# Kernel optimization log

Measured on AMD Instinct MI355X. Metric: run time of the kernel, lower is better.

## Reference

```python
import jax, jax.numpy as jnp
import numpy as np

B, T, D, H, K, ED = 4, 1024, 512, 8, 30, 128
HD = D // H
SCALE = HD ** -0.5


def _ln(x, g, b, eps=1e-5):
    m = jnp.mean(x, axis=-1, keepdims=True)
    v = jnp.var(x, axis=-1, keepdims=True)
    return (x - m) / jnp.sqrt(v + eps) * g + b


def setup_inputs() -> dict:
    key = jax.random.key(0)
    ks = jax.random.split(key, 16)
    s = 0.02
    return {
        "h_V": jax.random.normal(ks[0], (B, T, D), jnp.float32),
        "k": jax.random.normal(ks[1], (B, T, D), jnp.float32),
        "v": jax.random.normal(ks[2], (B, T, D), jnp.float32),
        "E": jax.random.normal(ks[3], (B, T, K, ED), jnp.float32),
        "bias": jax.random.normal(ks[4], (B, T, T), jnp.float32),
        "Wq": jax.random.normal(ks[5], (D, D), jnp.float32) * s,
        "bq": jnp.zeros((D,), jnp.float32),
        "Wk": jax.random.normal(ks[6], (D, D), jnp.float32) * s,
        "bk": jnp.zeros((D,), jnp.float32),
        "Wv": jax.random.normal(ks[7], (D, D), jnp.float32) * s,
        "bv": jnp.zeros((D,), jnp.float32),
        "Wo": jax.random.normal(ks[8], (D, D + ED), jnp.float32) * s,
        "bo": jnp.zeros((D,), jnp.float32),
        "t": jax.random.normal(ks[9], (1,), jnp.float32),
        "gn": jnp.ones((D,), jnp.float32),
        "bn": jnp.zeros((D,), jnp.float32),
        "w1": jax.random.normal(ks[10], (4 * D, D), jnp.float32) * s,
        "bw1": jnp.zeros((4 * D,), jnp.float32),
        "w2": jax.random.normal(ks[11], (D, 4 * D), jnp.float32) * s,
        "bw2": jnp.zeros((D,), jnp.float32),
        "gf": jnp.ones((D,), jnp.float32),
        "bf": jnp.zeros((D,), jnp.float32),
        "g2": jnp.ones((D,), jnp.float32),
        "b2": jnp.zeros((D,), jnp.float32),
        "E_idx": jax.random.randint(ks[12], (B, T, K), 0, T),
        "mask": jax.random.randint(ks[13], (B, T), 0, 2).astype(jnp.int32),
    }


def reference(h_V, k, v, E, bias, Wq, bq, Wk, bk, Wv, bv, Wo, bo, t, gn, bn, w1, bw1, w2, bw2, gf, bf, g2, b2, E_idx, mask):
    # q/k/v projections; q scaled by head_dim**-0.5 (as in torch: q *= scaling)
    q = (h_V @ Wq.T + bq) * SCALE
    kk = k @ Wk.T + bk
    vv = v @ Wv.T + bv
    qh = q.reshape(B, T, H, HD)
    kh = kk.reshape(B, T, H, HD)
    vh = vv.reshape(B, T, H, HD)
    # attention logits with additive pairwise bias, broadcast over heads
    aw = jnp.einsum('bthd,bshd->bhts', qh, kh) + bias[:, None, :, :]
    aw = jnp.where(mask[:, None, None, :] == 0, -1e9, aw)
    # h_attend temperature scaling
    aw = aw / (4.0 ** jnp.tanh(t[0]))
    p = jax.nn.softmax(aw, axis=-1)  # [B,H,T,S]
    attn = jnp.einsum('bhts,bshd->bthd', p, vh).reshape(B, T, D)
    # edge path: head-mean attention, gather neighbor weights, weighted edge sum
    ma = jnp.mean(p, axis=1)                       # [B,T,S]
    g = jnp.take_along_axis(ma, E_idx, axis=-1)    # [B,T,K]
    edge = (g[..., None] * E).sum(axis=2) / (g.sum(axis=-1, keepdims=True) + 1e-6)  # [B,T,ED]
    out = jnp.concatenate([attn, edge], axis=-1) @ Wo.T + bo
    h = _ln(h_V + out, gn, bn, eps=1e-5)
    # PositionwiseFeedForward: residual + LN(eps=1e-6)
    ff = jax.nn.gelu(h @ w1.T + bw1, approximate=False) @ w2.T + bw2
    dh = _ln(h + ff, gf, bf, eps=1e-6)
    return _ln(h + dh, g2, b2, eps=1e-5)
```

## Files before the change

### kernel.cpp

```cpp
#include <hip/hip_runtime.h>
#include <hip/hip_fp16.h>
#include <math.h>

#define B_ 4
#define T_ 1024
#define D_ 512
#define H_ 8
#define HD_ 64
#define KN 30
#define ED_ 128
#define DFF_ 2048
#define M_ 4096
#define BH_ 32

typedef _Float16 f16;
typedef __attribute__((ext_vector_type(8))) _Float16 f16x8;
typedef __attribute__((ext_vector_type(4))) _Float16 f16x4;
typedef __attribute__((ext_vector_type(4))) float f32x4;

#define MFMA16 __builtin_amdgcn_mfma_f32_16x16x32_f16
#define LOG2E 1.44269504088896f

__device__ __forceinline__ f16x8 ld8(const f16* p){ return *reinterpret_cast<const f16x8*>(p); }

__device__ __forceinline__ void gld16(const void* g, void* l){
  __builtin_amdgcn_global_load_lds((const __attribute__((address_space(1))) void*)g,
                                   (__attribute__((address_space(3))) void*)l, 16, 0, 0);
}

struct CvtJobs {
  const float* s[9];
  f16* d[9];
  int start[10];
};

__global__ __launch_bounds__(256) void cvt9_kernel(CvtJobs J){
  const int blk = blockIdx.x;
  int j = 0;
  while (j < 8 && blk >= J.start[j+1]) ++j;
  const int i = (blk - J.start[j])*256 + threadIdx.x;
  float4 v = reinterpret_cast<const float4*>(J.s[j])[i];
  union { f16 h[4]; ushort4 u; } o;
  o.h[0]=(f16)v.x; o.h[1]=(f16)v.y; o.h[2]=(f16)v.z; o.h[3]=(f16)v.w;
  reinterpret_cast<ushort4*>(J.d[j])[i] = o.u;
}

__global__ __launch_bounds__(256) void biasprep_kernel(
    const float* __restrict__ bias, const int* __restrict__ mask,
    const float* __restrict__ tsc, f16* __restrict__ biasT)
{
  const int TT = blockIdx.x*256 + threadIdx.x;
  const int G = TT >> 4, l16 = TT & 15;
  const int qg = G & 1, step = (G >> 1) & 1, ws = (G >> 2) & 3;
  const int c = (G >> 4) & 7, tb = (G >> 7) & 31, bi = G >> 12;
  const float s = exp2f(-2.0f*tanhf(tsc[0]))*LOG2E;
  const int t  = tb*32 + qg*16 + l16;
  const int s0 = c*128 + ws*32 + step*16;
  const float* bp = bias + ((size_t)bi*T_ + t)*T_ + s0;
  const int*   mp = mask + bi*T_ + s0;
  union { f16 h[16]; f16x8 v8[2]; } o;
#pragma unroll
  for (int i = 0; i < 16; i += 4){
    float4 v = *reinterpret_cast<const float4*>(bp + i);
    int4  mm = *reinterpret_cast<const int4*>(mp + i);
    float x[4] = {v.x,v.y,v.z,v.w};
    int  m4[4] = {mm.x,mm.y,mm.z,mm.w};
#pragma unroll
    for (int j = 0; j < 4; ++j){
      float tv = (x[j] + (m4[j] ? 0.f : -60000.f))*s;
      o.h[i+j] = (f16)fmaxf(tv, -60000.f);
    }
  }
  f16* op = biasT + (size_t)G*256 + l16*16;
  reinterpret_cast<f16x8*>(op)[0] = o.v8[0];
  reinterpret_cast<f16x8*>(op)[1] = o.v8[1];
}

template<int EPI>
__global__ __launch_bounds__(256,2) void gemm_tile(
    const f16* __restrict__ X, const f16* __restrict__ W,
    const float* __restrict__ bias, void* __restrict__ outp,
    int Kd, int ldo, int nbN)
{
  __shared__ f16 As[128*64];
  __shared__ f16 Bs[128*64];
  const int nwg = gridDim.x;
  const int bid = blockIdx.x;
  const int swz = (bid & 7)*(nwg >> 3) + (bid >> 3);
  const int mb = swz / nbN, nb = swz - mb*nbN;
  const int rb = mb*128, cb = nb*128;
  const int tid = threadIdx.x;
  const int w = tid >> 6, lane = tid & 63;
  const int l16 = lane & 15, l4 = lane >> 4;
  const int wr = w >> 1, wc = w & 1;
  const int key = l16 & 7;

  f32x4 acc[4][4];
#pragma unroll
  for (int m = 0; m < 4; ++m)
#pragma unroll
    for (int n = 0; n < 4; ++n) acc[m][n] = (f32x4){0.f,0.f,0.f,0.f};

  for (int k0 = 0; k0 < Kd; k0 += 64){
#pragma unroll
    for (int i = 0; i < 4; ++i){
      const int cidx = i*256 + w*64 + lane;
      const int r = cidx >> 3, p = cidx & 7;
      gld16(X + (size_t)(rb + r)*Kd + k0 + ((p ^ (r & 7)) << 3),
            &As[(i*256 + w*64)*8]);
      gld16(W + (size_t)(cb + r)*Kd + k0 + ((p ^ (r & 7)) << 3),
            &Bs[(i*256 + w*64)*8]);
    }
    __syncthreads();
#pragma unroll
    for (int kk = 0; kk < 2; ++kk){
      f16x8 a[4], b[4];
#pragma unroll
      for (int m = 0; m < 4; ++m)
        a[m] = ld8(&As[(wr*64 + m*16 + l16)*64 + (((kk*4 + l4) ^ key) << 3)]);
#pragma unroll
      for (int n = 0; n < 4; ++n)
        b[n] = ld8(&Bs[(wc*64 + n*16 + l16)*64 + (((kk*4 + l4) ^ key) << 3)]);
#pragma unroll
      for (int m = 0; m < 4; ++m)
#pragma unroll
        for (int n = 0; n < 4; ++n)
          acc[m][n] = MFMA16(a[m], b[n], acc[m][n], 0,0,0);
    }
    __syncthreads();
  }

#pragma unroll
  for (int n = 0; n < 4; ++n){
    const int col = cb + wc*64 + n*16 + l16;
    const float bv = bias[col];
#pragma unroll
    for (int m = 0; m < 4; ++m){
#pragma unroll
      for (int j = 0; j < 4; ++j){
        const int row = rb + wr*64 + m*16 + l4*4 + j;
        float v = acc[m][n][j] + bv;
        if (EPI == 1){
          v = 0.5f*v*(1.0f + erff(v*0.70710678118654752f));
          ((f16*)outp)[(size_t)row*ldo + col] = (f16)v;
        } else {
          ((float*)outp)[(size_t)row*ldo + col] = v;
        }
      }
    }
  }
}

template<int EPI>
__global__ __launch_bounds__(256,2) void gemm_n64(
    const f16* __restrict__ X, const f16* __restrict__ W,
    const float* __restrict__ bias, void* __restrict__ outp,
    int Kd, int ldo, int nbN)
{
  __shared__ f16 As[128*64];
  __shared__ f16 Bs[64*64];
  const int nwg = gridDim.x;
  const int bid = blockIdx.x;
  const int swz = (bid & 7)*(nwg >> 3) + (bid >> 3);
  const int mb = swz / nbN, nb = swz - mb*nbN;
  const int rb = mb*128, cb = nb*64;
  const int tid = threadIdx.x;
  const int w = tid >> 6, lane = tid & 63;
  const int l16 = lane & 15, l4 = lane >> 4;
  const int wr = w >> 1, wc = w & 1;
  const int key = l16 & 7;

  f32x4 acc[4][2];
#pragma unroll
  for (int m = 0; m < 4; ++m)
#pragma unroll
    for (int n = 0; n < 2; ++n) acc[m][n] = (f32x4){0.f,0.f,0.f,0.f};

  for (int k0 = 0; k0 < Kd; k0 += 64){
#pragma unroll
    for (int i = 0; i < 4; ++i){
      const int cidx = i*256 + w*64 + lane;
      const int r = cidx >> 3, p = cidx & 7;
      gld16(X + (size_t)(rb + r)*Kd + k0 + ((p ^ (r & 7)) << 3),
            &As[(i*256 + w*64)*8]);
    }
#pragma unroll
    for (int i = 0; i < 2; ++i){
      const int cidx = i*256 + w*64 + lane;
      const int r = cidx >> 3, p = cidx & 7;
      gld16(W + (size_t)(cb + r)*Kd + k0 + ((p ^ (r & 7)) << 3),
            &Bs[(i*256 + w*64)*8]);
    }
    __syncthreads();
#pragma unroll
    for (int kk = 0; kk < 2; ++kk){
      f16x8 a[4], b[2];
#pragma unroll
      for (int m = 0; m < 4; ++m)
        a[m] = ld8(&As[(wr*64 + m*16 + l16)*64 + (((kk*4 + l4) ^ key) << 3)]);
#pragma unroll
      for (int n = 0; n < 2; ++n)
        b[n] = ld8(&Bs[(wc*32 + n*16 + l16)*64 + (((kk*4 + l4) ^ key) << 3)]);
#pragma unroll
      for (int m = 0; m < 4; ++m)
#pragma unroll
        for (int n = 0; n < 2; ++n)
          acc[m][n] = MFMA16(a[m], b[n], acc[m][n], 0,0,0);
    }
    __syncthreads();
  }

#pragma unroll
  for (int n = 0; n < 2; ++n){
    const int col = cb + wc*32 + n*16 + l16;
    const float bv = bias[col];
#pragma unroll
    for (int m = 0; m < 4; ++m){
#pragma unroll
      for (int j = 0; j < 4; ++j){
        const int row = rb + wr*64 + m*16 + l4*4 + j;
        float v = acc[m][n][j] + bv;
        if (EPI == 1){
          v = 0.5f*v*(1.0f + erff(v*0.70710678118654752f));
          ((f16*)outp)[(size_t)row*ldo + col] = (f16)v;
        } else {
          ((float*)outp)[(size_t)row*ldo + col] = v;
        }
      }
    }
  }
}

__global__ __launch_bounds__(256,2) void qkv_tile(
    const f16* __restrict__ hV, const f16* __restrict__ kI, const f16* __restrict__ vI,
    const f16* __restrict__ Wq, const f16* __restrict__ Wk, const f16* __restrict__ Wv,
    const float* __restrict__ bq, const float* __restrict__ bk, const float* __restrict__ bv,
    const float* __restrict__ tsc,
    f16* __restrict__ qo, f16* __restrict__ ko, f16* __restrict__ vT)
{
  __shared__ f16 As[128*32];
  __shared__ f16 Bs[128*32];
  const int bid = blockIdx.x;
  const int swz = (bid & 7)*48 + (bid >> 3);
  const int g = swz >> 7;
  const int r = swz & 127;
  const int mb = r >> 2, nb = r & 3;
  const f16* X  = (g == 0) ? hV : ((g == 1) ? kI : vI);
  const f16* W  = (g == 0) ? Wq : ((g == 1) ? Wk : Wv);
  const float* bias = (g == 0) ? bq : ((g == 1) ? bk : bv);
  const int rb = mb*128, cb = nb*128;
  const int tid = threadIdx.x;
  const int w = tid >> 6, lane = tid & 63;
  const int l16 = lane & 15, l4 = lane >> 4;
  const int wr = w >> 1, wc = w & 1;
  const int sr = lane >> 2, sc = (lane & 3)*8;
  const f16* Ax0 = X + (size_t)(rb + w*16 + sr)*D_ + sc;
  const f16* Ax1 = X + (size_t)(rb + 64 + w*16 + sr)*D_ + sc;
  const f16* Bx0 = W + (size_t)(cb + w*16 + sr)*D_ + sc;
  const f16* Bx1 = W + (size_t)(cb + 64 + w*16 + sr)*D_ + sc;
  f16* Ad0 = &As[(w*16)*32];
  f16* Ad1 = &As[(64 + w*16)*32];
  f16* Bd0 = &Bs[(w*16)*32];
  f16* Bd1 = &Bs[(64 + w*16)*32];

  f32x4 acc[4][4];
#pragma unroll
  for (int m = 0; m < 4; ++m)
#pragma unroll
    for (int n = 0; n < 4; ++n) acc[m][n] = (f32x4){0.f,0.f,0.f,0.f};

  for (int k0 = 0; k0 < D_; k0 += 32){
    gld16(Ax0 + k0, Ad0);
    gld16(Ax1 + k0, Ad1);
    gld16(Bx0 + k0, Bd0);
    gld16(Bx1 + k0, Bd1);
    __syncthreads();
    f16x8 a[4], b[4];
#pragma unroll
    for (int m = 0; m < 4; ++m) a[m] = ld8(&As[(wr*64 + m*16 + l16)*32 + l4*8]);
#pragma unroll
    for (int n = 0; n < 4; ++n) b[n] = ld8(&Bs[(wc*64 + n*16 + l16)*32 + l4*8]);
#pragma unroll
    for (int m = 0; m < 4; ++m)
#pragma unroll
      for (int n = 0; n < 4; ++n)
        acc[m][n] = MFMA16(a[m], b[n], acc[m][n], 0,0,0);
    __syncthreads();
  }

  const float qs = exp2f(-2.0f*tanhf(tsc[0]))*LOG2E*0.125f;
  const float scale = (g == 0) ? qs : 1.0f;
  f16* out = (g == 0) ? qo : ko;
#pragma unroll
  for (int n = 0; n < 4; ++n){
    const int col = cb + wc*64 + n*16 + l16;
    const float bv = bias[col];
#pragma unroll
    for (int m = 0; m < 4; ++m){
#pragma unroll
      for (int j = 0; j < 4; ++j){
        const int row = rb + wr*64 + m*16 + l4*4 + j;
        const float v = (acc[m][n][j] + bv)*scale;
        if (g < 2){
          out[(size_t)row*D_ + col] = (f16)v;
        } else {
          const int b = row >> 10, t = row & (T_-1);
          const int h = col >> 6,  dl = col & (HD_-1);
          vT[(((size_t)b*H_ + h)*HD_ + dl)*T_ + t] = (f16)v;
        }
      }
    }
  }
}

__global__ __launch_bounds__(512,4) void attn_fused(
    const f16* __restrict__ q, const f16* __restrict__ k, const f16* __restrict__ vT,
    const f16* __restrict__ biasT, const int* __restrict__ eidx,
    f16* __restrict__ X2, float* __restrict__ gpart)
{
  __shared__ f16 Sb[16384];
  __shared__ f16 Pc[32*128];
  const int bid = blockIdx.x;
  const int swz = (bid & 7)*128 + (bid >> 3);
  const int bh = swz >> 5, tb = swz & 31;
  const int bi = bh >> 3, h = bh & 7;
  const int t0 = tb*32;
  const int tid = threadIdx.x, w = tid >> 6, lane = tid & 63;
  const int qg = w >> 2, ws = w & 3;
  const int l16 = lane & 15, l4 = lane >> 4;
  const int key = l16 & 7;

  const f16* qp = q + (size_t)(bi*T_ + t0 + qg*16 + l16)*D_ + h*HD_ + l4*8;
  const f16x8 q0 = ld8(qp), q1 = ld8(qp + 32);
  const int tl = tid & 255;
  int ga_r, ga_kk, ga_id, gb_r = 0, gb_kk = 0, gb_id = -1;
  ga_r = tl/KN; ga_kk = tl - ga_r*KN;
  ga_id = eidx[((size_t)(bi*T_ + t0 + qg*16 + ga_r))*KN + ga_kk];
  if (tl + 256 < 16*KN){
    gb_r = (tl+256)/KN; gb_kk = (tl+256) - gb_r*KN;
    gb_id = eidx[((size_t)(bi*T_ + t0 + qg*16 + gb_r))*KN + gb_kk];
  }

  const f16* kg = k + (size_t)(bi*T_)*D_ + h*HD_;
  const f16* vg = vT + (size_t)bh*HD_*T_;
  const f16* bb = biasT + (size_t)(bi*32 + tb)*32768 + ws*1024 + qg*256 + l16*16 + l4*4;

  auto stageK = [&](int c, int slot){
#pragma unroll
    for (int i = 0; i < 2; ++i){
      const int cidx = i*512 + w*64 + lane;
      const int r = cidx >> 3, p = cidx & 7;
      gld16(kg + (size_t)(c*128 + r)*D_ + ((p ^ (r & 7)) << 3),
            &Sb[slot*8192 + (i*512 + w*64)*8]);
    }
  };
  auto stageV = [&](int sc, int slot){
#pragma unroll
    for (int i = 0; i < 2; ++i){
      const int cidx = i*512 + w*64 + lane;
      const int r = cidx >> 4, p = cidx & 15;
      gld16(vg + (size_t)r*T_ + sc*128 + ((p ^ (r & 7)) << 3),
            &Sb[slot*8192 + (i*512 + w*64)*8]);
    }
  };

  f32x4 acc[16];
  stageK(0, 0);
#pragma unroll
  for (int c = 0; c < 8; ++c){
    if (c < 7) stageK(c+1, (c+1)&1);
    if (c < 7) asm volatile("s_waitcnt vmcnt(2)" ::: "memory");
    else       asm volatile("s_waitcnt vmcnt(0)" ::: "memory");
    __builtin_amdgcn_sched_barrier(0);
    __builtin_amdgcn_s_barrier();
    __builtin_amdgcn_sched_barrier(0);
    const int base = (c&1)*8192;
#pragma unroll
    for (int step = 0; step < 2; ++step){
      const int rr = ws*32 + step*16 + l16;
      f32x4 a = {0.f,0.f,0.f,0.f};
      a = MFMA16(ld8(&Sb[base + rr*64 + ((l4 ^ key) << 3)]),       q0, a, 0,0,0);
      a = MFMA16(ld8(&Sb[base + rr*64 + (((4 + l4) ^ key) << 3)]), q1, a, 0,0,0);
      const f16x4 bf = *reinterpret_cast<const f16x4*>(bb + c*4096 + step*512);
#pragma unroll
      for (int j = 0; j < 4; ++j) a[j] += (float)bf[j];
      acc[c*2 + step] = a;
    }
    __builtin_amdgcn_s_barrier();
  }

  float* redf = (float*)Sb;
  float m = -3.4e38f;
#pragma unroll
  for (int c = 0; c < 16; ++c)
#pragma unroll
    for (int j = 0; j < 4; ++j) m = fmaxf(m, acc[c][j]);
  m = fmaxf(m, __shfl_xor(m, 16));
  m = fmaxf(m, __shfl_xor(m, 32));
  if (lane < 16) redf[(qg*4 + ws)*16 + lane] = m;
  __syncthreads();
  m = fmaxf(fmaxf(redf[(qg*4+0)*16 + l16], redf[(qg*4+1)*16 + l16]),
            fmaxf(redf[(qg*4+2)*16 + l16], redf[(qg*4+3)*16 + l16]));
  float l = 0.f;
#pragma unroll
  for (int c = 0; c < 16; ++c)
#pragma unroll
    for (int j = 0; j < 4; ++j){
      const float e = exp2f(acc[c][j] - m);
      l += e;
      acc[c][j] = e;
    }
  l += __shfl_xor(l, 16);
  l += __shfl_xor(l, 32);
  if (lane < 16) redf[128 + (qg*4 + ws)*16 + lane] = l;
  __syncthreads();
  const float lrq = redf[128 + (qg*4+0)*16 + l16] + redf[128 + (qg*4+1)*16 + l16]
                  + redf[128 + (qg*4+2)*16 + l16] + redf[128 + (qg*4+3)*16 + l16];
  __syncthreads();
  const float lr_a = __shfl(lrq, ga_r);
  const float lr_b = __shfl(lrq, gb_r);

  f32x4 oo0 = {0.f,0.f,0.f,0.f}, oo1 = oo0, oo2 = oo0, oo3 = oo0;
  stageV(0, 0);
#pragma unroll
  for (int sc = 0; sc < 8; ++sc){
#pragma unroll
    for (int step = 0; step < 2; ++step){
      const int slb = ws*32 + step*16 + l4*4;
      f16x4 pp;
#pragma unroll
      for (int j = 0; j < 4; ++j) pp[j] = (f16)acc[sc*2 + step][j];
      *reinterpret_cast<f16x4*>(
          &Pc[(qg*16 + l16)*128 + (((slb >> 3) ^ key) << 3) + (slb & 7)]) = pp;
    }
    if (sc < 7) stageV(sc+1, (sc+1)&1);
    if (sc < 7) asm volatile("s_waitcnt vmcnt(2) lgkmcnt(0)" ::: "memory");
    else        asm volatile("s_waitcnt vmcnt(0) lgkmcnt(0)" ::: "memory");
    __builtin_amdgcn_sched_barrier(0);
    __builtin_amdgcn_s_barrier();
    __builtin_amdgcn_sched_barrier(0);
    const int base = (sc&1)*8192;
    const int vrow = (ws*16 + l16)*128;
#pragma unroll
    for (int grp = 0; grp < 4; ++grp){
      const int ch = (grp*4 + l4) ^ key;
      const f16x8 pa = ld8(&Pc[(qg*16 + l16)*128 + (ch << 3)]);
      const f16x8 vb = ld8(&Sb[base + vrow + (ch << 3)]);
      if (grp == 0)      oo0 = MFMA16(pa, vb, oo0, 0,0,0);
      else if (grp == 1) oo1 = MFMA16(pa, vb, oo1, 0,0,0);
      else if (grp == 2) oo2 = MFMA16(pa, vb, oo2, 0,0,0);
      else               oo3 = MFMA16(pa, vb, oo3, 0,0,0);
    }
    if ((ga_id >> 7) == sc){
      const int r = qg*16 + ga_r;
      const int sl = ga_id & 127;
      const float pv = (float)Pc[r*128 + ((((sl >> 3) ^ (r & 7)) << 3) | (sl & 7))];
      gpart[((size_t)bh*T_ + t0 + r)*KN + ga_kk] = pv/lr_a*0.125f;
    }
    if (gb_id >= 0 && (gb_id >> 7) == sc){
      const int r = qg*16 + gb_r;
      const int sl = gb_id & 127;
      const float pv = (float)Pc[r*128 + ((((sl >> 3) ^ (r & 7)) << 3) | (sl & 7))];
      gpart[((size_t)bh*T_ + t0 + r)*KN + gb_kk] = pv/lr_b*0.125f;
    }
    __builtin_amdgcn_s_barrier();
  }
  const f32x4 o = (oo0 + oo1) + (oo2 + oo3);

#pragma unroll
  for (int j = 0; j < 4; ++j){
    const float lr = __shfl(lrq, l4*4 + j);
    const int t = t0 + qg*16 + l4*4 + j;
    X2[((size_t)(bi*T_ + t))*640 + h*HD_ + ws*16 + l16] = (f16)(o[j]/lr);
  }
}

__global__ __launch_bounds__(128) void edge_kernel(
    const float* __restrict__ gpart, const float* __restrict__ E, f16* __restrict__ X2)
{
  __shared__ float gl[KN];
  __shared__ float ginv;
  const int bt = blockIdx.x;
  const int bi = bt >> 10, tt = bt & 1023;
  const int t = threadIdx.x;
  if (t < KN){
    float s = 0.f;
#pragma unroll
    for (int hh = 0; hh < H_; ++hh)
      s += gpart[((size_t)(bi*H_ + hh)*T_ + tt)*KN + t];
    gl[t] = s;
  }
  __syncthreads();
  if (t == 0){
    float s = 0.f;
#pragma unroll
    for (int i = 0; i < KN; ++i) s += gl[i];
    ginv = 1.0f/(s + 1e-6f);
  }
  __syncthreads();
  float acc = 0.f;
  const float* Ep = E + (size_t)bt*KN*ED_ + t;
#pragma unroll 5
  for (int kk = 0; kk < KN; ++kk) acc += gl[kk]*Ep[(size_t)kk*ED_];
  X2[(size_t)bt*640 + 512 + t] = (f16)(acc*ginv);
}

__device__ __forceinline__ float block_sum(float v, float* sbuf){
  for (int o = 32; o; o >>= 1) v += __shfl_down(v, o);
  __syncthreads();
  if ((threadIdx.x & 63) == 0) sbuf[threadIdx.x >> 6] = v;
  __syncthreads();
  return sbuf[0]+sbuf[1]+sbuf[2]+sbuf[3];
}

__global__ __launch_bounds__(256) void ln1_kernel(
    const float* __restrict__ hV, const float* __restrict__ hraw,
    const float* __restrict__ gn, const float* __restrict__ bn,
    float* __restrict__ hf, f16* __restrict__ hh)
{
  __shared__ float sbuf[4];
  const int r = blockIdx.x, t = threadIdx.x;
  const size_t base = (size_t)r*D_;
  float x0 = hV[base+t]     + hraw[base+t];
  float x1 = hV[base+t+256] + hraw[base+t+256];
  float s = block_sum(x0+x1, sbuf);
  const float mean = s*(1.f/512.f);
  float d0 = x0-mean, d1 = x1-mean;
  float vs = block_sum(d0*d0+d1*d1, sbuf);
  const float rstd = rsqrtf(vs*(1.f/512.f) + 1e-5f);
  float y0 = d0*rstd*gn[t]     + bn[t];
  float y1 = d1*rstd*gn[t+256] + bn[t+256];
  hf[base+t]     = y0;  hh[base+t]     = (f16)y0;
  hf[base+t+256] = y1;  hh[base+t+256] = (f16)y1;
}

__global__ __launch_bounds__(256) void final_kernel(
    const float* __restrict__ hf, const float* __restrict__ ffr,
    const float* __restrict__ gf, const float* __restrict__ bfv,
    const float* __restrict__ g2, const float* __restrict__ b2,
    float* __restrict__ out)
{
  __shared__ float sbuf[4];
  const int r = blockIdx.x, t = threadIdx.x;
  const size_t base = (size_t)r*D_;
  const float h0 = hf[base+t], h1 = hf[base+t+256];
  float x0 = h0 + ffr[base+t], x1 = h1 + ffr[base+t+256];
  float s = block_sum(x0+x1, sbuf);
  float mean = s*(1.f/512.f);
  float d0 = x0-mean, d1 = x1-mean;
  float vs = block_sum(d0*d0+d1*d1, sbuf);
  float rstd = rsqrtf(vs*(1.f/512.f) + 1e-6f);
  const float dh0 = d0*rstd*gf[t]     + bfv[t];
  const float dh1 = d1*rstd*gf[t+256] + bfv[t+256];
  const float y0 = h0 + dh0, y1 = h1 + dh1;
  s = block_sum(y0+y1, sbuf);
  mean = s*(1.f/512.f);
  d0 = y0-mean; d1 = y1-mean;
  vs = block_sum(d0*d0+d1*d1, sbuf);
  rstd = rsqrtf(vs*(1.f/512.f) + 1e-5f);
  out[base+t]     = d0*rstd*g2[t]     + b2[t];
  out[base+t+256] = d1*rstd*g2[t+256] + b2[t+256];
}

extern "C" void kernel_launch(void* const* d_in, const int* in_sizes, int n_in,
                              void* d_out, int out_size, void* d_ws, size_t ws_size,
                              hipStream_t stream)
{
  (void)in_sizes; (void)n_in; (void)out_size;
  const float* h_V  = (const float*)d_in[0];
  const float* kin  = (const float*)d_in[1];
  const float* vin  = (const float*)d_in[2];
  const float* E    = (const float*)d_in[3];
  const float* bias = (const float*)d_in[4];
  const float* Wq   = (const float*)d_in[5];
  const float* bq   = (const float*)d_in[6];
  const float* Wk   = (const float*)d_in[7];
  const float* bk   = (const float*)d_in[8];
  const float* Wv   = (const float*)d_in[9];
  const float* bv   = (const float*)d_in[10];
  const float* Wo   = (const float*)d_in[11];
  const float* bo   = (const float*)d_in[12];
  const float* tsc  = (const float*)d_in[13];
  const float* gn   = (const float*)d_in[14];
  const float* bn   = (const float*)d_in[15];
  const float* w1   = (const float*)d_in[16];
  const float* bw1  = (const float*)d_in[17];
  const float* w2   = (const float*)d_in[18];
  const float* bw2  = (const float*)d_in[19];
  const float* gf   = (const float*)d_in[20];
  const float* bfv  = (const float*)d_in[21];
  const float* g2   = (const float*)d_in[22];
  const float* b2   = (const float*)d_in[23];
  const int*   Eidx = (const int*)d_in[24];
  const int*   mask = (const int*)d_in[25];
  float* out = (float*)d_out;

  char* wsb = (char*)d_ws;
  size_t off = 0;
  auto alloc = [&](size_t bytes) -> void* {
    void* pp = wsb + off; off += (bytes + 255) & ~(size_t)255; return pp;
  };
  f16* hVb  = (f16*)alloc((size_t)M_*D_*2);
  f16* kbI  = (f16*)alloc((size_t)M_*D_*2);
  f16* vbI  = (f16*)alloc((size_t)M_*D_*2);
  f16* Wqb  = (f16*)alloc((size_t)D_*D_*2);
  f16* Wkb  = (f16*)alloc((size_t)D_*D_*2);
  f16* Wvb  = (f16*)alloc((size_t)D_*D_*2);
  f16* Wob  = (f16*)alloc((size_t)D_*(D_+ED_)*2);
  f16* w1b  = (f16*)alloc((size_t)DFF_*D_*2);
  f16* w2b  = (f16*)alloc((size_t)D_*DFF_*2);
  f16* qb   = (f16*)alloc((size_t)M_*D_*2);
  f16* kb   = (f16*)alloc((size_t)M_*D_*2);
  f16* vT   = (f16*)alloc((size_t)M_*D_*2);
  f16* biasT= (f16*)alloc((size_t)B_*T_*T_*2);
  f16* X2   = (f16*)alloc((size_t)M_*640*2);
  float* gpart = (float*)alloc((size_t)BH_*T_*KN*4);
  float* hraw = (float*)alloc((size_t)M_*D_*4);
  float* hf   = (float*)alloc((size_t)M_*D_*4);
  f16*   hh   = (f16*)alloc((size_t)M_*D_*2);
  f16*   ff1  = (f16*)alloc((size_t)M_*DFF_*2);
  if (ws_size < off) return;
  float* ffraw = hraw;

  {
    CvtJobs J;
    const float* srcs[9] = {h_V, kin, vin, Wq, Wk, Wv, Wo, w1, w2};
    f16* dsts[9] = {hVb, kbI, vbI, Wqb, Wkb, Wvb, Wob, w1b, w2b};
    const int n4s[9] = {M_*D_/4, M_*D_/4, M_*D_/4, D_*D_/4, D_*D_/4, D_*D_/4,
                        D_*(D_+ED_)/4, DFF_*D_/4, D_*DFF_/4};
    int cum = 0;
    for (int i = 0; i < 9; ++i){
      J.s[i] = srcs[i]; J.d[i] = dsts[i]; J.start[i] = cum;
      cum += n4s[i]/256;
    }
    J.start[9] = cum;
    cvt9_kernel<<<cum,256,0,stream>>>(J);
  }
  biasprep_kernel<<<1024,256,0,stream>>>(bias, mask, tsc, biasT);

  qkv_tile<<<384,256,0,stream>>>(hVb, kbI, vbI, Wqb, Wkb, Wvb, bq, bk, bv, tsc, qb, kb, vT);

  attn_fused<<<1024,512,0,stream>>>(qb, kb, vT, biasT, Eidx, X2, gpart);

  edge_kernel<<<M_,128,0,stream>>>(gpart, E, X2);

  gemm_n64<2><<<256,256,0,stream>>>(X2, Wob, bo, hraw, D_+ED_, D_, 8);
  ln1_kernel<<<M_,256,0,stream>>>(h_V, hraw, gn, bn, hf, hh);

  gemm_tile<1><<<512,256,0,stream>>>(hh, w1b, bw1, ff1, D_, DFF_, 16);
  gemm_n64<2><<<256,256,0,stream>>>(ff1, w2b, bw2, ffraw, DFF_, D_, 8);

  final_kernel<<<M_,256,0,stream>>>(hf, ffraw, gf, bfv, g2, b2, out);
}
```

Before: 168.1 us.

## Prefetch bias fragments, defer gpart stores, and store GEMM/LN intermediates in fp16

The bias prep kernel is re-laid-out so each thread writes one 8-wide fp16 vector. The attention kernel loads all eight bias fragments for its slice into registers up front, so they are no longer read inside the S loop, and it writes the gathered edge weights once after the loop. The Wo and FFN2 GEMM outputs and the LN1 output become fp16, and the separate fp32 copy of h is dropped, which cuts intermediate memory traffic. In exchange the attention kernel uses more registers, and the residual/LayerNorm chain loses precision because h is now carried in fp16.

```diff
diff --git a/kernel.cpp b/kernel.cpp
--- a/kernel.cpp
+++ b/kernel.cpp
@@ -49,31 +49,28 @@
     const float* __restrict__ bias, const int* __restrict__ mask,
     const float* __restrict__ tsc, f16* __restrict__ biasT)
 {
-  const int TT = blockIdx.x*256 + threadIdx.x;
-  const int G = TT >> 4, l16 = TT & 15;
-  const int qg = G & 1, step = (G >> 1) & 1, ws = (G >> 2) & 3;
-  const int c = (G >> 4) & 7, tb = (G >> 7) & 31, bi = G >> 12;
+  const int u = blockIdx.x*256 + threadIdx.x;
+  const int l4 = u & 3, l16 = (u >> 2) & 15, qg = (u >> 6) & 1;
+  const int ws = (u >> 7) & 3, c = (u >> 9) & 7, tb = (u >> 12) & 31, bi = u >> 17;
   const float s = exp2f(-2.0f*tanhf(tsc[0]))*LOG2E;
   const int t  = tb*32 + qg*16 + l16;
-  const int s0 = c*128 + ws*32 + step*16;
+  const int s0 = c*128 + ws*32 + l4*4;
   const float* bp = bias + ((size_t)bi*T_ + t)*T_ + s0;
   const int*   mp = mask + bi*T_ + s0;
-  union { f16 h[16]; f16x8 v8[2]; } o;
-#pragma unroll
-  for (int i = 0; i < 16; i += 4){
-    float4 v = *reinterpret_cast<const float4*>(bp + i);
-    int4  mm = *reinterpret_cast<const int4*>(mp + i);
+  union { f16 h[8]; f16x8 v8; } o;
+#pragma unroll
+  for (int st = 0; st < 2; ++st){
+    float4 v = *reinterpret_cast<const float4*>(bp + st*16);
+    int4  mm = *reinterpret_cast<const int4*>(mp + st*16);
     float x[4] = {v.x,v.y,v.z,v.w};
     int  m4[4] = {mm.x,mm.y,mm.z,mm.w};
 #pragma unroll
     for (int j = 0; j < 4; ++j){
       float tv = (x[j] + (m4[j] ? 0.f : -60000.f))*s;
-      o.h[i+j] = (f16)fmaxf(tv, -60000.f);
-    }
-  }
-  f16* op = biasT + (size_t)G*256 + l16*16;
-  reinterpret_cast<f16x8*>(op)[0] = o.v8[0];
-  reinterpret_cast<f16x8*>(op)[1] = o.v8[1];
+      o.h[st*4 + j] = (f16)fmaxf(tv, -60000.f);
+    }
+  }
+  *reinterpret_cast<f16x8*>(biasT + (size_t)u*8) = o.v8;
 }
 
 template<int EPI>
@@ -140,12 +137,8 @@
       for (int j = 0; j < 4; ++j){
         const int row = rb + wr*64 + m*16 + l4*4 + j;
         float v = acc[m][n][j] + bv;
-        if (EPI == 1){
-          v = 0.5f*v*(1.0f + erff(v*0.70710678118654752f));
-          ((f16*)outp)[(size_t)row*ldo + col] = (f16)v;
-        } else {
-          ((float*)outp)[(size_t)row*ldo + col] = v;
-        }
+        if (EPI == 1) v = 0.5f*v*(1.0f + erff(v*0.70710678118654752f));
+        ((f16*)outp)[(size_t)row*ldo + col] = (f16)v;
       }
     }
   }
@@ -220,12 +213,8 @@
       for (int j = 0; j < 4; ++j){
         const int row = rb + wr*64 + m*16 + l4*4 + j;
         float v = acc[m][n][j] + bv;
-        if (EPI == 1){
-          v = 0.5f*v*(1.0f + erff(v*0.70710678118654752f));
-          ((f16*)outp)[(size_t)row*ldo + col] = (f16)v;
-        } else {
-          ((float*)outp)[(size_t)row*ldo + col] = v;
-        }
+        if (EPI == 1) v = 0.5f*v*(1.0f + erff(v*0.70710678118654752f));
+        ((f16*)outp)[(size_t)row*ldo + col] = (f16)v;
       }
     }
   }
@@ -332,6 +321,10 @@
 
   const f16* qp = q + (size_t)(bi*T_ + t0 + qg*16 + l16)*D_ + h*HD_ + l4*8;
   const f16x8 q0 = ld8(qp), q1 = ld8(qp + 32);
+  const f16* bb = biasT + (size_t)(bi*32 + tb)*32768 + ws*1024 + qg*512 + l16*32 + l4*8;
+  f16x8 bfr[8];
+#pragma unroll
+  for (int c = 0; c < 8; ++c) bfr[c] = ld8(bb + c*4096);
   const int tl = tid & 255;
   int ga_r, ga_kk, ga_id, gb_r = 0, gb_kk = 0, gb_id = -1;
   ga_r = tl/KN; ga_kk = tl - ga_r*KN;
@@ -343,7 +336,6 @@
 
   const f16* kg = k + (size_t)(bi*T_)*D_ + h*HD_;
   const f16* vg = vT + (size_t)bh*HD_*T_;
-  const f16* bb = biasT + (size_t)(bi*32 + tb)*32768 + ws*1024 + qg*256 + l16*16 + l4*4;
 
   auto stageK = [&](int c, int slot){
 #pragma unroll
@@ -381,9 +373,8 @@
       f32x4 a = {0.f,0.f,0.f,0.f};
       a = MFMA16(ld8(&Sb[base + rr*64 + ((l4 ^ key) << 3)]),       q0, a, 0,0,0);
       a = MFMA16(ld8(&Sb[base + rr*64 + (((4 + l4) ^ key) << 3)]), q1, a, 0,0,0);
-      const f16x4 bf = *reinterpret_cast<const f16x4*>(bb + c*4096 + step*512);
-#pragma unroll
-      for (int j = 0; j < 4; ++j) a[j] += (float)bf[j];
+#pragma unroll
+      for (int j = 0; j < 4; ++j) a[j] += (float)bfr[c][step*4 + j];
       acc[c*2 + step] = a;
     }
     __builtin_amdgcn_s_barrier();
@@ -421,6 +412,7 @@
   const float lr_b = __shfl(lrq, gb_r);
 
   f32x4 oo0 = {0.f,0.f,0.f,0.f}, oo1 = oo0, oo2 = oo0, oo3 = oo0;
+  float pva = 0.f, pvb = 0.f;
   stageV(0, 0);
 #pragma unroll
   for (int sc = 0; sc < 8; ++sc){
@@ -454,18 +446,20 @@
     if ((ga_id >> 7) == sc){
       const int r = qg*16 + ga_r;
       const int sl = ga_id & 127;
-      const float pv = (float)Pc[r*128 + ((((sl >> 3) ^ (r & 7)) << 3) | (sl & 7))];
-      gpart[((size_t)bh*T_ + t0 + r)*KN + ga_kk] = pv/lr_a*0.125f;
+      pva = (float)Pc[r*128 + ((((sl >> 3) ^ (r & 7)) << 3) | (sl & 7))];
     }
     if (gb_id >= 0 && (gb_id >> 7) == sc){
       const int r = qg*16 + gb_r;
       const int sl = gb_id & 127;
-      const float pv = (float)Pc[r*128 + ((((sl >> 3) ^ (r & 7)) << 3) | (sl & 7))];
-      gpart[((size_t)bh*T_ + t0 + r)*KN + gb_kk] = pv/lr_b*0.125f;
+      pvb = (float)Pc[r*128 + ((((sl >> 3) ^ (r & 7)) << 3) | (sl & 7))];
     }
     __builtin_amdgcn_s_barrier();
   }
   const f32x4 o = (oo0 + oo1) + (oo2 + oo3);
+
+  gpart[((size_t)bh*T_ + t0 + qg*16 + ga_r)*KN + ga_kk] = pva/lr_a*0.125f;
+  if (gb_id >= 0)
+    gpart[((size_t)bh*T_ + t0 + qg*16 + gb_r)*KN + gb_kk] = pvb/lr_b*0.125f;
 
 #pragma unroll
   for (int j = 0; j < 4; ++j){
@@ -514,28 +508,26 @@
 }
 
 __global__ __launch_bounds__(256) void ln1_kernel(
-    const float* __restrict__ hV, const float* __restrict__ hraw,
+    const float* __restrict__ hV, const f16* __restrict__ hraw,
     const float* __restrict__ gn, const float* __restrict__ bn,
-    float* __restrict__ hf, f16* __restrict__ hh)
+    f16* __restrict__ hh)
 {
   __shared__ float sbuf[4];
   const int r = blockIdx.x, t = threadIdx.x;
   const size_t base = (size_t)r*D_;
-  float x0 = hV[base+t]     + hraw[base+t];
-  float x1 = hV[base+t+256] + hraw[base+t+256];
+  float x0 = hV[base+t]     + (float)hraw[base+t];
+  float x1 = hV[base+t+256] + (float)hraw[base+t+256];
   float s = block_sum(x0+x1, sbuf);
   const float mean = s*(1.f/512.f);
   float d0 = x0-mean, d1 = x1-mean;
   float vs = block_sum(d0*d0+d1*d1, sbuf);
   const float rstd = rsqrtf(vs*(1.f/512.f) + 1e-5f);
-  float y0 = d0*rstd*gn[t]     + bn[t];
-  float y1 = d1*rstd*gn[t+256] + bn[t+256];
-  hf[base+t]     = y0;  hh[base+t]     = (f16)y0;
-  hf[base+t+256] = y1;  hh[base+t+256] = (f16)y1;
+  hh[base+t]     = (f16)(d0*rstd*gn[t]     + bn[t]);
+  hh[base+t+256] = (f16)(d1*rstd*gn[t+256] + bn[t+256]);
 }
 
 __global__ __launch_bounds__(256) void final_kernel(
-    const float* __restrict__ hf, const float* __restrict__ ffr,
+    const f16* __restrict__ hh, const f16* __restrict__ ffr,
     const float* __restrict__ gf, const float* __restrict__ bfv,
     const float* __restrict__ g2, const float* __restrict__ b2,
     float* __restrict__ out)
@@ -543,8 +535,8 @@
   __shared__ float sbuf[4];
   const int r = blockIdx.x, t = threadIdx.x;
   const size_t base = (size_t)r*D_;
-  const float h0 = hf[base+t], h1 = hf[base+t+256];
-  float x0 = h0 + ffr[base+t], x1 = h1 + ffr[base+t+256];
+  const float h0 = (float)hh[base+t], h1 = (float)hh[base+t+256];
+  float x0 = h0 + (float)ffr[base+t], x1 = h1 + (float)ffr[base+t+256];
   float s = block_sum(x0+x1, sbuf);
   float mean = s*(1.f/512.f);
   float d0 = x0-mean, d1 = x1-mean;
@@ -615,12 +607,11 @@
   f16* biasT= (f16*)alloc((size_t)B_*T_*T_*2);
   f16* X2   = (f16*)alloc((size_t)M_*640*2);
   float* gpart = (float*)alloc((size_t)BH_*T_*KN*4);
-  float* hraw = (float*)alloc((size_t)M_*D_*4);
-  float* hf   = (float*)alloc((size_t)M_*D_*4);
-  f16*   hh   = (f16*)alloc((size_t)M_*D_*2);
-  f16*   ff1  = (f16*)alloc((size_t)M_*DFF_*2);
+  f16* hraw = (f16*)alloc((size_t)M_*D_*2);
+  f16* hh   = (f16*)alloc((size_t)M_*D_*2);
+  f16* ff1  = (f16*)alloc((size_t)M_*DFF_*2);
   if (ws_size < off) return;
-  float* ffraw = hraw;
+  f16* ffraw = hraw;
 
   {
     CvtJobs J;
@@ -636,7 +627,7 @@
     J.start[9] = cum;
     cvt9_kernel<<<cum,256,0,stream>>>(J);
   }
-  biasprep_kernel<<<1024,256,0,stream>>>(bias, mask, tsc, biasT);
+  biasprep_kernel<<<2048,256,0,stream>>>(bias, mask, tsc, biasT);
 
   qkv_tile<<<384,256,0,stream>>>(hVb, kbI, vbI, Wqb, Wkb, Wvb, bq, bk, bv, tsc, qb, kb, vT);
 
@@ -645,10 +636,10 @@
   edge_kernel<<<M_,128,0,stream>>>(gpart, E, X2);
 
   gemm_n64<2><<<256,256,0,stream>>>(X2, Wob, bo, hraw, D_+ED_, D_, 8);
-  ln1_kernel<<<M_,256,0,stream>>>(h_V, hraw, gn, bn, hf, hh);
+  ln1_kernel<<<M_,256,0,stream>>>(h_V, hraw, gn, bn, hh);
 
   gemm_tile<1><<<512,256,0,stream>>>(hh, w1b, bw1, ff1, D_, DFF_, 16);
   gemm_n64<2><<<256,256,0,stream>>>(ff1, w2b, bw2, ffraw, DFF_, D_, 8);
 
-  final_kernel<<<M_,256,0,stream>>>(hf, ffraw, gf, bfv, g2, b2, out);
-}
+  final_kernel<<<M_,256,0,stream>>>(hh, ffraw, gf, bfv, g2, b2, out);
+}
```

Measured after the change: 162.3 us. 3.4% less time.
